# Kernel optimization log

Hardware: AMD Instinct MI355X
Metric: run time of the kernel (lower is better)

The kernel has to match this reference:

```python
import jax, jax.numpy as jnp
import numpy as np

H, D = 4, 32          # heads, per-head dim (= hidden_channels)
HD = H * D            # concat width fed between layers
L = 2                 # num HGT layers
OUT = 128             # final output dim
SCALE = 1.0 / np.sqrt(D)


def _seg_softmax(score, seg, n):
    # segment softmax over incoming edges per destination node, per head
    mx = jax.ops.segment_max(score, seg, num_segments=n)
    ex = jnp.exp(score - mx[seg])
    den = jax.ops.segment_sum(ex, seg, num_segments=n)
    return ex / den[seg]


def _hgt_side(q_dst, k_src, v_src, src, dst, a_rel, m_rel, p_rel, n_dst):
    # k/v: [N_src,H,D]; a_rel,m_rel: [H,D,D]; p_rel: [H]
    k_t = jnp.einsum('ehd,hdf->ehf', k_src[src], a_rel)          # [E,H,D]
    score = (q_dst[dst] * k_t).sum(-1) * p_rel * SCALE           # [E,H]
    alpha = _seg_softmax(score, dst, n_dst)                      # [E,H]
    v_t = jnp.einsum('ehd,hdf->ehf', v_src[src], m_rel)          # [E,H,D]
    return jax.ops.segment_sum(alpha[..., None] * v_t, dst, num_segments=n_dst)


def _forward(x_m, x_g, W_in_m, b_in_m, W_in_g, b_in_g,
             Wk_m, bk_m, Wq_m, bq_m, Wv_m, bv_m,
             Wk_g, bk_g, Wq_g, bq_g, Wv_g, bv_g,
             a_mg, m_mg, p_mg, a_gm, m_gm, p_gm,
             Wa_m, ba_m, Wa_g, ba_g, skip_m, skip_g,
             W_out_m, b_out_m, W_out_g, b_out_g,
             edge_mg_src, edge_mg_dst, edge_gm_src, edge_gm_dst):
    Nm, Ng = x_m.shape[0], x_g.shape[0]
    # per-node-type input projection
    h_m = x_m @ W_in_m + b_in_m                                  # [Nm,HD]
    h_g = x_g @ W_in_g + b_in_g                                  # [Ng,HD]
    for l in range(L):
        k_m = (h_m @ Wk_m[l] + bk_m[l]).reshape(Nm, H, D)
        q_m = (h_m @ Wq_m[l] + bq_m[l]).reshape(Nm, H, D)
        v_m = (h_m @ Wv_m[l] + bv_m[l]).reshape(Nm, H, D)
        k_g = (h_g @ Wk_g[l] + bk_g[l]).reshape(Ng, H, D)
        q_g = (h_g @ Wq_g[l] + bq_g[l]).reshape(Ng, H, D)
        v_g = (h_g @ Wv_g[l] + bv_g[l]).reshape(Ng, H, D)
        agg_g = _hgt_side(q_g, k_m, v_m, edge_mg_src, edge_mg_dst,
                          a_mg[l], m_mg[l], p_mg[l], Ng)         # [Ng,H,D]
        agg_m = _hgt_side(q_m, k_g, v_g, edge_gm_src, edge_gm_dst,
                          a_gm[l], m_gm[l], p_gm[l], Nm)         # [Nm,H,D]
        o_m = jax.nn.gelu(agg_m.reshape(Nm, HD), approximate=False) @ Wa_m[l] + ba_m[l]
        o_g = jax.nn.gelu(agg_g.reshape(Ng, HD), approximate=False) @ Wa_g[l] + ba_g[l]
        bm = jax.nn.sigmoid(skip_m[l])
        bg = jax.nn.sigmoid(skip_g[l])
        h_m = jax.nn.elu(bm * o_m + (1.0 - bm) * h_m)            # HGTConv skip, then model-level ELU
        h_g = jax.nn.elu(bg * o_g + (1.0 - bg) * h_g)
    out_m = h_m @ W_out_m + b_out_m                              # [Nm,OUT]
    out_g = h_g @ W_out_g + b_out_g                              # [Ng,OUT]
    return jnp.concatenate([out_m, out_g], axis=0)               # [Nm+Ng,OUT]


def setup_inputs() -> dict:
    key = jax.random.key(0)
    ks = iter(jax.random.split(key, 64))
    Nm, Ng, E = 100000, 20000, 500000
    Fm, Fg = 20, 50
    def n(shape, s=0.05):
        return jax.random.normal(next(ks), shape, jnp.float32) * s
    inp = {
        'x_m': n((Nm, Fm), 1.0), 'x_g': n((Ng, Fg), 1.0),
        'W_in_m': n((Fm, HD)), 'b_in_m': jnp.zeros((HD,), jnp.float32),
        'W_in_g': n((Fg, HD)), 'b_in_g': jnp.zeros((HD,), jnp.float32),
        'Wk_m': n((L, HD, HD)), 'bk_m': jnp.zeros((L, HD), jnp.float32),
        'Wq_m': n((L, HD, HD)), 'bq_m': jnp.zeros((L, HD), jnp.float32),
        'Wv_m': n((L, HD, HD)), 'bv_m': jnp.zeros((L, HD), jnp.float32),
        'Wk_g': n((L, HD, HD)), 'bk_g': jnp.zeros((L, HD), jnp.float32),
        'Wq_g': n((L, HD, HD)), 'bq_g': jnp.zeros((L, HD), jnp.float32),
        'Wv_g': n((L, HD, HD)), 'bv_g': jnp.zeros((L, HD), jnp.float32),
        'a_mg': n((L, H, D, D)), 'm_mg': n((L, H, D, D)),
        'p_mg': jnp.ones((L, H), jnp.float32),
        'a_gm': n((L, H, D, D)), 'm_gm': n((L, H, D, D)),
        'p_gm': jnp.ones((L, H), jnp.float32),
        'Wa_m': n((L, HD, HD)), 'ba_m': jnp.zeros((L, HD), jnp.float32),
        'Wa_g': n((L, HD, HD)), 'ba_g': jnp.zeros((L, HD), jnp.float32),
        'skip_m': jnp.ones((L,), jnp.float32), 'skip_g': jnp.ones((L,), jnp.float32),
        'W_out_m': n((HD, OUT)), 'b_out_m': jnp.zeros((OUT,), jnp.float32),
        'W_out_g': n((HD, OUT)), 'b_out_g': jnp.zeros((OUT,), jnp.float32),
        'edge_mg_src': jax.random.randint(next(ks), (E,), 0, Nm, jnp.int32),
        'edge_mg_dst': jax.random.randint(next(ks), (E,), 0, Ng, jnp.int32),
        'edge_gm_src': jax.random.randint(next(ks), (E,), 0, Ng, jnp.int32),
        'edge_gm_dst': jax.random.randint(next(ks), (E,), 0, Nm, jnp.int32),
    }
    return inp


def reference(x_m, x_g, W_in_m, b_in_m, W_in_g, b_in_g,
              Wk_m, bk_m, Wq_m, bq_m, Wv_m, bv_m,
              Wk_g, bk_g, Wq_g, bq_g, Wv_g, bv_g,
              a_mg, m_mg, p_mg, a_gm, m_gm, p_gm,
              Wa_m, ba_m, Wa_g, ba_g, skip_m, skip_g,
              W_out_m, b_out_m, W_out_g, b_out_g,
              edge_mg_src, edge_mg_dst, edge_gm_src, edge_gm_dst):
    return _forward(x_m, x_g, W_in_m, b_in_m, W_in_g, b_in_g,
                    Wk_m, bk_m, Wq_m, bq_m, Wv_m, bv_m,
                    Wk_g, bk_g, Wq_g, bq_g, Wv_g, bv_g,
                    a_mg, m_mg, p_mg, a_gm, m_gm, p_gm,
                    Wa_m, ba_m, Wa_g, ba_g, skip_m, skip_g,
                    W_out_m, b_out_m, W_out_g, b_out_g,
                    edge_mg_src, edge_mg_dst, edge_gm_src, edge_gm_dst)
```

## Files before the change

kernel.cpp:

```cpp
#include <hip/hip_runtime.h>
#include <hip/hip_bf16.h>

#define SCALE_F 0.17677669529663688f

typedef __attribute__((ext_vector_type(8)))  short bfrag;
typedef __attribute__((ext_vector_type(16))) float facc;

__device__ __forceinline__ float lo16(unsigned u){ return __uint_as_float(u << 16); }
__device__ __forceinline__ float hi16(unsigned u){ return __uint_as_float(u & 0xffff0000u); }
__device__ __forceinline__ float bu2f(unsigned short u){ return __uint_as_float((unsigned)u << 16); }
__device__ __forceinline__ unsigned short f2bu(float f){
    __hip_bfloat16 h = __float2bfloat16(f);
    return *reinterpret_cast<unsigned short*>(&h);
}
__device__ __forceinline__ void storeC(float* p, float v){ *p = v; }
__device__ __forceinline__ void storeC(__hip_bfloat16* p, float v){ *p = __float2bfloat16(v); }

__global__ void hist_k(const int* __restrict__ dst, int* __restrict__ cnt, int E, int Nd){
    int e = blockIdx.x*256 + threadIdx.x;
    if (e >= E) return;
    int d = dst[e];
    if ((unsigned)d < (unsigned)Nd) atomicAdd(&cnt[d], 1);
}

__global__ void scan_block_k(const int* __restrict__ cnt, int* __restrict__ incl,
                             int* __restrict__ bsum, int N){
    __shared__ int sh[256];
    int tid = threadIdx.x;
    int i = blockIdx.x*256 + tid;
    int v = (i < N) ? cnt[i] : 0;
    sh[tid] = v;
    __syncthreads();
    for (int off = 1; off < 256; off <<= 1){
        int t = (tid >= off) ? sh[tid-off] : 0;
        __syncthreads();
        sh[tid] += t;
        __syncthreads();
    }
    if (i < N) incl[i] = sh[tid];
    if (tid == 255) bsum[blockIdx.x] = sh[255];
}

__global__ void scan_top_k(int* __restrict__ bsum, int nb){
    __shared__ int sh[512];
    int tid = threadIdx.x;
    int v = (tid < nb) ? bsum[tid] : 0;
    sh[tid] = v;
    __syncthreads();
    for (int off = 1; off < 512; off <<= 1){
        int t = (tid >= off) ? sh[tid-off] : 0;
        __syncthreads();
        sh[tid] += t;
        __syncthreads();
    }
    if (tid < nb) bsum[tid] = sh[tid] - v;
}

__global__ void finalize_k(const int* __restrict__ incl, const int* __restrict__ cnt,
                           const int* __restrict__ boff, int* __restrict__ indptr,
                           int N, int E){
    int i = blockIdx.x*256 + threadIdx.x;
    if (i > N) return;
    if (i == N){ indptr[N] = E; return; }
    indptr[i] = boff[i >> 8] + incl[i] - cnt[i];
}

__global__ void scatter_k(const int* __restrict__ src, const int* __restrict__ dst,
                          const int* __restrict__ indptr, int* __restrict__ cur,
                          int* __restrict__ csr, int E, int Nd){
    int e = blockIdx.x*256 + threadIdx.x;
    if (e >= E) return;
    int d = dst[e];
    if ((unsigned)d >= (unsigned)Nd) return;
    int p = indptr[d] + atomicAdd(&cur[d], 1);
    csr[p] = src[e];
}

template<int K>
__global__ __launch_bounds__(128) void in_proj_k(const float* __restrict__ x,
                                                 const float* __restrict__ W,
                                                 const float* __restrict__ b,
                                                 unsigned short* __restrict__ h, int N){
    constexpr int KP4 = (K + 3)/4, KP = KP4*4;
    int j = threadIdx.x;
    float wreg[KP];
    #pragma unroll
    for (int k = 0; k < KP; ++k) wreg[k] = (k < K) ? W[k*128 + j] : 0.f;
    float bj = b[j];
    __shared__ float xs[8][KP];
    for (int base = blockIdx.x*8; base < N; base += gridDim.x*8){
        __syncthreads();
        for (int t = threadIdx.x; t < 8*KP; t += 128){
            int r = t / KP, k = t - r*KP;
            int row = base + r;
            xs[r][k] = (row < N && k < K) ? x[(size_t)row*K + k] : 0.f;
        }
        __syncthreads();
        #pragma unroll
        for (int r = 0; r < 8; ++r){
            int row = base + r;
            if (row >= N) break;
            float acc = bj;
            #pragma unroll
            for (int kk = 0; kk < KP4; ++kk){
                float4 xv = *(const float4*)(&xs[r][kk*4]);
                acc += xv.x*wreg[kk*4] + xv.y*wreg[kk*4+1]
                     + xv.z*wreg[kk*4+2] + xv.w*wreg[kk*4+3];
            }
            h[(size_t)row*128 + j] = f2bu(acc);
        }
    }
}

__global__ __launch_bounds__(128) void build_wf2_k(
    const float* __restrict__ Wq0, const float* __restrict__ bq0,
    const float* __restrict__ Wk0, const float* __restrict__ bk0,
    const float* __restrict__ Wv0, const float* __restrict__ bv0,
    const float* __restrict__ ar0, const float* __restrict__ mr0,
    unsigned short* __restrict__ Wto0, float* __restrict__ bfo0,
    const float* __restrict__ Wq1, const float* __restrict__ bq1,
    const float* __restrict__ Wk1, const float* __restrict__ bk1,
    const float* __restrict__ Wv1, const float* __restrict__ bv1,
    const float* __restrict__ ar1, const float* __restrict__ mr1,
    unsigned short* __restrict__ Wto1, float* __restrict__ bfo1){
    bool sA = (blockIdx.y == 0);
    const float* Wq = sA ? Wq0 : Wq1;  const float* bq = sA ? bq0 : bq1;
    const float* Wk = sA ? Wk0 : Wk1;  const float* bk = sA ? bk0 : bk1;
    const float* Wv = sA ? Wv0 : Wv1;  const float* bvp = sA ? bv0 : bv1;
    const float* ar = sA ? ar0 : ar1;  const float* mr = sA ? mr0 : mr1;
    unsigned short* Wt = sA ? Wto0 : Wto1;
    float* bf = sA ? bfo0 : bfo1;
    int j = blockIdx.x, row = threadIdx.x;
    int part = j >> 7, f = j & 127, hh = f >> 5, ff = f & 31;
    float v;
    if (part == 0) v = Wq[row*128 + f];
    else {
        const float* Wx  = (part == 1) ? Wk : Wv;
        const float* rel = (part == 1) ? ar : mr;
        float s = 0.f;
        #pragma unroll
        for (int d = 0; d < 32; ++d)
            s += Wx[row*128 + hh*32 + d] * rel[hh*1024 + d*32 + ff];
        v = s;
    }
    Wt[(size_t)j*128 + row] = f2bu(v);
    if (row == 0){
        float bb;
        if (part == 0) bb = bq[f];
        else {
            const float* bx  = (part == 1) ? bk : bvp;
            const float* rel = (part == 1) ? ar : mr;
            float s = 0.f;
            for (int d = 0; d < 32; ++d)
                s += bx[hh*32 + d] * rel[hh*1024 + d*32 + ff];
            bb = s;
        }
        bf[j] = bb;
    }
}

__global__ void transpose6_k(const float* a0, const float* a1, const float* a2,
                             const float* a3, const float* a4, const float* a5,
                             unsigned short* d0, unsigned short* d1, unsigned short* d2,
                             unsigned short* d3, unsigned short* d4, unsigned short* d5){
    int y = blockIdx.y;
    const float* S = (y==0)?a0:(y==1)?a1:(y==2)?a2:(y==3)?a3:(y==4)?a4:a5;
    unsigned short* D = (y==0)?d0:(y==1)?d1:(y==2)?d2:(y==3)?d3:(y==4)?d4:d5;
    int idx = blockIdx.x*256 + threadIdx.x;
    int n = idx >> 7, k = idx & 127;
    D[idx] = f2bu(S[k*128 + n]);
}

template<typename CT, int MODE>
__global__ __launch_bounds__(256) void mfma_gemm2(
    const unsigned short* __restrict__ A0, const unsigned short* __restrict__ Wt0,
    const float* __restrict__ bias0, CT* __restrict__ C0, unsigned short* __restrict__ H0,
    int N0, const float* __restrict__ skip0,
    const unsigned short* __restrict__ A1, const unsigned short* __restrict__ Wt1,
    const float* __restrict__ bias1, CT* __restrict__ C1, unsigned short* __restrict__ H1,
    int N1, const float* __restrict__ skip1,
    int ldc, int nblk0){
    bool s0 = ((int)blockIdx.x < nblk0);
    const unsigned short* A  = s0 ? A0 : A1;
    const unsigned short* Wt = s0 ? Wt0 : Wt1;
    const float* bias = s0 ? bias0 : bias1;
    CT* C = s0 ? C0 : C1;
    unsigned short* H = s0 ? H0 : H1;
    int N = s0 ? N0 : N1;
    const float* skip = s0 ? skip0 : skip1;
    int bx = s0 ? blockIdx.x : (blockIdx.x - nblk0);

    __shared__ unsigned short As[64][136];
    __shared__ unsigned short Bs[128][136];
    int tid = threadIdx.x;
    int rb = bx*64, cb = blockIdx.y*128;
    #pragma unroll
    for (int ph = 0; ph < 4; ++ph){
        int c = ph*256 + tid;
        int r = c >> 4, off = (c & 15)*8;
        uint4 v = make_uint4(0,0,0,0);
        if (rb + r < N) v = ((const uint4*)(A + (size_t)(rb + r)*128))[c & 15];
        *(uint4*)(&As[r][off]) = v;
    }
    #pragma unroll
    for (int ph = 0; ph < 8; ++ph){
        int c = ph*256 + tid;
        int r = c >> 4, off = (c & 15)*8;
        uint4 v = ((const uint4*)(Wt + (size_t)(cb + r)*128))[c & 15];
        *(uint4*)(&Bs[r][off]) = v;
    }
    __syncthreads();
    int w = tid >> 6, lane = tid & 63;
    int wr = (w >> 1)*32, wc = (w & 1)*64;
    int m = lane & 31, quad = lane >> 5;
    facc acc0, acc1;
    #pragma unroll
    for (int i = 0; i < 16; ++i){ acc0[i] = 0.f; acc1[i] = 0.f; }
    const unsigned short* ap  = &As[wr + m][quad*8];
    const unsigned short* bp0 = &Bs[wc + m][quad*8];
    const unsigned short* bp1 = &Bs[wc + 32 + m][quad*8];
    #pragma unroll
    for (int kc = 0; kc < 8; ++kc){
        bfrag a  = *(const bfrag*)(ap  + kc*16);
        bfrag b0 = *(const bfrag*)(bp0 + kc*16);
        bfrag b1 = *(const bfrag*)(bp1 + kc*16);
        acc0 = __builtin_amdgcn_mfma_f32_32x32x16_bf16(a, b0, acc0, 0, 0, 0);
        acc1 = __builtin_amdgcn_mfma_f32_32x32x16_bf16(a, b1, acc1, 0, 0, 0);
    }
    int col0 = cb + wc + m, col1 = col0 + 32;
    float bias0v = bias[col0], bias1v = bias[col1];
    float bm = 0.f;
    if (MODE == 2) bm = 1.f/(1.f + __expf(-skip[0]));
    #pragma unroll
    for (int r = 0; r < 16; ++r){
        int lrow = wr + 4*quad + (r & 3) + 8*(r >> 2);
        int grow = rb + lrow;
        if (grow >= N) continue;
        float o0 = acc0[r] + bias0v;
        float o1 = acc1[r] + bias1v;
        if (MODE == 0){
            storeC(&C[(size_t)grow*ldc + col0], o0);
            storeC(&C[(size_t)grow*ldc + col1], o1);
        } else {
            size_t i0 = (size_t)grow*128 + col0, i1 = (size_t)grow*128 + col1;
            float v0 = bm*o0 + (1.f - bm)*bu2f(H[i0]);
            float v1 = bm*o1 + (1.f - bm)*bu2f(H[i1]);
            v0 = (v0 > 0.f) ? v0 : expm1f(v0);
            v1 = (v1 > 0.f) ? v1 : expm1f(v1);
            H[i0] = f2bu(v0);
            H[i1] = f2bu(v1);
        }
    }
}

__global__ __launch_bounds__(256) void edge_attn2_k(
    const int* __restrict__ ipA, const int* __restrict__ csrA,
    const unsigned short* __restrict__ qdA, const unsigned short* __restrict__ qsA,
    const float* __restrict__ pA, unsigned* __restrict__ aggA, int NdA,
    const int* __restrict__ ipB, const int* __restrict__ csrB,
    const unsigned short* __restrict__ qdB, const unsigned short* __restrict__ qsB,
    const float* __restrict__ pB, unsigned* __restrict__ aggB, int NdB,
    int nblkA){
    bool sA = ((int)blockIdx.x < nblkA);
    const int* ip  = sA ? ipA : ipB;
    const int* csr = sA ? csrA : csrB;
    const unsigned* qd = (const unsigned*)(sA ? qdA : qdB);
    const unsigned* qs = (const unsigned*)(sA ? qsA : qsB);
    const float* p = sA ? pA : pB;
    unsigned* agg = sA ? aggA : aggB;
    int Nd = sA ? NdA : NdB;
    int bx = sA ? blockIdx.x : (blockIdx.x - nblkA);
    int wid  = (bx << 2) | (threadIdx.x >> 6);
    int lane = threadIdx.x & 63;
    if (wid >= Nd) return;
    float ph = p[lane >> 4] * SCALE_F;
    unsigned qu = qd[(size_t)wid*192 + lane];
    float q0 = lo16(qu), q1 = hi16(qu);
    int beg = ip[wid], end = ip[wid + 1];
    float den = 0.f, a0 = 0.f, a1 = 0.f;
    int i = beg;
    for (; i + 1 < end; i += 2){
        int s0 = csr[i], s1 = csr[i+1];
        const unsigned* b0 = qs + (size_t)s0*192;
        const unsigned* b1 = qs + (size_t)s1*192;
        unsigned ku0 = b0[64 + lane], vu0 = b0[128 + lane];
        unsigned ku1 = b1[64 + lane], vu1 = b1[128 + lane];
        float t0 = q0*lo16(ku0) + q1*hi16(ku0);
        float t1 = q0*lo16(ku1) + q1*hi16(ku1);
        t0 += __shfl_xor(t0, 1);  t1 += __shfl_xor(t1, 1);
        t0 += __shfl_xor(t0, 2);  t1 += __shfl_xor(t1, 2);
        t0 += __shfl_xor(t0, 4);  t1 += __shfl_xor(t1, 4);
        t0 += __shfl_xor(t0, 8);  t1 += __shfl_xor(t1, 8);
        float e0 = __expf(t0*ph), e1 = __expf(t1*ph);
        den += e0 + e1;
        a0 += e0*lo16(vu0) + e1*lo16(vu1);
        a1 += e0*hi16(vu0) + e1*hi16(vu1);
    }
    if (i < end){
        int s0 = csr[i];
        const unsigned* b0 = qs + (size_t)s0*192;
        unsigned ku0 = b0[64 + lane], vu0 = b0[128 + lane];
        float t0 = q0*lo16(ku0) + q1*hi16(ku0);
        t0 += __shfl_xor(t0, 1);
        t0 += __shfl_xor(t0, 2);
        t0 += __shfl_xor(t0, 4);
        t0 += __shfl_xor(t0, 8);
        float e0 = __expf(t0*ph);
        den += e0; a0 += e0*lo16(vu0); a1 += e0*hi16(vu0);
    }
    float inv = (den > 0.f) ? 1.f/den : 0.f;
    float o0 = a0*inv, o1 = a1*inv;
    o0 = 0.5f*o0*(1.f + erff(o0*0.70710678118654752f));
    o1 = 0.5f*o1*(1.f + erff(o1*0.70710678118654752f));
    agg[(size_t)wid*64 + lane] = (unsigned)f2bu(o0) | ((unsigned)f2bu(o1) << 16);
}

extern "C" void kernel_launch(void* const* d_in, const int* in_sizes, int n_in,
                              void* d_out, int out_size, void* d_ws, size_t ws_size,
                              hipStream_t stream){
    typedef const float* FP;
    FP x_m = (FP)d_in[0], x_g = (FP)d_in[1];
    FP W_in_m = (FP)d_in[2], b_in_m = (FP)d_in[3], W_in_g = (FP)d_in[4], b_in_g = (FP)d_in[5];
    FP Wk_m = (FP)d_in[6],  bk_m = (FP)d_in[7],  Wq_m = (FP)d_in[8],  bq_m = (FP)d_in[9];
    FP Wv_m = (FP)d_in[10], bv_m = (FP)d_in[11];
    FP Wk_g = (FP)d_in[12], bk_g = (FP)d_in[13], Wq_g = (FP)d_in[14], bq_g = (FP)d_in[15];
    FP Wv_g = (FP)d_in[16], bv_g = (FP)d_in[17];
    FP a_mg = (FP)d_in[18], m_mg = (FP)d_in[19], p_mg = (FP)d_in[20];
    FP a_gm = (FP)d_in[21], m_gm = (FP)d_in[22], p_gm = (FP)d_in[23];
    FP Wa_m = (FP)d_in[24], ba_m = (FP)d_in[25], Wa_g = (FP)d_in[26], ba_g = (FP)d_in[27];
    FP skip_m = (FP)d_in[28], skip_g = (FP)d_in[29];
    FP W_out_m = (FP)d_in[30], b_out_m = (FP)d_in[31], W_out_g = (FP)d_in[32], b_out_g = (FP)d_in[33];
    const int* e_mg_src = (const int*)d_in[34];
    const int* e_mg_dst = (const int*)d_in[35];
    const int* e_gm_src = (const int*)d_in[36];
    const int* e_gm_dst = (const int*)d_in[37];

    const int Nm = in_sizes[0] / 20;
    const int Ng = in_sizes[1] / 50;
    const int E1 = in_sizes[34];
    const int E2 = in_sizes[36];

    char* wp = (char*)d_ws;
    auto alloc = [&](size_t bytes) -> char* {
        char* r = wp; wp += (bytes + 255) & ~(size_t)255; return r;
    };
    unsigned short* h_m   = (unsigned short*)alloc((size_t)Nm*128*2);
    unsigned short* h_g   = (unsigned short*)alloc((size_t)Ng*128*2);
    unsigned short* agg_m = (unsigned short*)alloc((size_t)Nm*128*2);
    unsigned short* agg_g = (unsigned short*)alloc((size_t)Ng*128*2);
    unsigned short* qkv_m = (unsigned short*)alloc((size_t)Nm*384*2);
    unsigned short* qkv_g = (unsigned short*)alloc((size_t)Ng*384*2);
    unsigned short* Wtf   = (unsigned short*)alloc((size_t)4*49152*2);
    float*          bfv   = (float*)alloc((size_t)4*384*4);
    unsigned short* Wta   = (unsigned short*)alloc((size_t)4*16384*2);
    unsigned short* Wtout = (unsigned short*)alloc((size_t)2*16384*2);
    int* indptr_g = (int*)alloc((size_t)(Ng+1)*4);
    int* csr_mg   = (int*)alloc((size_t)E1*4);
    int* indptr_m = (int*)alloc((size_t)(Nm+1)*4);
    int* csr_gm   = (int*)alloc((size_t)E2*4);
    int maxN = Nm > Ng ? Nm : Ng;
    int* cnt  = (int*)alloc((size_t)maxN*4);
    int* cur  = (int*)alloc((size_t)maxN*4);
    int* cnt2 = (int*)alloc((size_t)maxN*4);
    int* cur2 = (int*)alloc((size_t)maxN*4);
    int* incl = (int*)alloc((size_t)maxN*4);
    int* bsum = (int*)alloc(512*4);

    size_t used = (size_t)(wp - (char*)d_ws);
    if (used > ws_size){
        hipMemsetAsync(d_out, 0, (size_t)out_size*4, stream);
        return;
    }
    hipMemsetAsync(cnt, 0, (size_t)((char*)cur2 - (char*)cnt) + (size_t)maxN*4, stream);

    auto buildCSR = [&](const int* esrc, const int* edst, int E, int Nd,
                        int* indptr, int* csr, int* c0, int* c1){
        hist_k<<<(E + 255)/256, 256, 0, stream>>>(edst, c0, E, Nd);
        int nb = (Nd + 255)/256;
        scan_block_k<<<nb, 256, 0, stream>>>(c0, incl, bsum, Nd);
        scan_top_k<<<1, 512, 0, stream>>>(bsum, nb);
        finalize_k<<<(Nd + 256)/256 + 1, 256, 0, stream>>>(incl, c0, bsum, indptr, Nd, E);
        scatter_k<<<(E + 255)/256, 256, 0, stream>>>(esrc, edst, indptr, c1, csr, E, Nd);
    };
    buildCSR(e_mg_src, e_mg_dst, E1, Ng, indptr_g, csr_mg, cnt, cur);
    buildCSR(e_gm_src, e_gm_dst, E2, Nm, indptr_m, csr_gm, cnt2, cur2);

    transpose6_k<<<dim3(64, 6), 256, 0, stream>>>(
        Wa_m, Wa_g, Wa_m + 16384, Wa_g + 16384, W_out_m, W_out_g,
        Wta, Wta + 16384, Wta + 32768, Wta + 49152, Wtout, Wtout + 16384);
    for (int l = 0; l < 2; ++l){
        build_wf2_k<<<dim3(384, 2), 128, 0, stream>>>(
            Wq_m + l*16384, bq_m + l*128, Wk_m + l*16384, bk_m + l*128,
            Wv_m + l*16384, bv_m + l*128, a_mg + l*4096, m_mg + l*4096,
            Wtf + (size_t)(l*2+0)*49152, bfv + (l*2+0)*384,
            Wq_g + l*16384, bq_g + l*128, Wk_g + l*16384, bk_g + l*128,
            Wv_g + l*16384, bv_g + l*128, a_gm + l*4096, m_gm + l*4096,
            Wtf + (size_t)(l*2+1)*49152, bfv + (l*2+1)*384);
    }

    int gim = (Nm + 7)/8; if (gim > 2048) gim = 2048;
    int gig = (Ng + 7)/8; if (gig > 2048) gig = 2048;
    in_proj_k<20><<<gim, 128, 0, stream>>>(x_m, W_in_m, b_in_m, h_m, Nm);
    in_proj_k<50><<<gig, 128, 0, stream>>>(x_g, W_in_g, b_in_g, h_g, Ng);

    int gxm = (Nm + 63)/64, gxg = (Ng + 63)/64;
    int nbA = (Ng + 3)/4, nbB = (Nm + 3)/4;

    for (int l = 0; l < 2; ++l){
        mfma_gemm2<__hip_bfloat16, 0><<<dim3(gxm + gxg, 3), 256, 0, stream>>>(
            h_m, Wtf + (size_t)(l*2+0)*49152, bfv + (l*2+0)*384,
            (__hip_bfloat16*)qkv_m, nullptr, Nm, nullptr,
            h_g, Wtf + (size_t)(l*2+1)*49152, bfv + (l*2+1)*384,
            (__hip_bfloat16*)qkv_g, nullptr, Ng, nullptr,
            384, gxm);

        edge_attn2_k<<<nbA + nbB, 256, 0, stream>>>(
            indptr_g, csr_mg, qkv_g, qkv_m, p_mg + l*4, (unsigned*)agg_g, Ng,
            indptr_m, csr_gm, qkv_m, qkv_g, p_gm + l*4, (unsigned*)agg_m, Nm,
            nbA);

        mfma_gemm2<float, 2><<<dim3(gxm + gxg, 1), 256, 0, stream>>>(
            agg_m, Wta + (size_t)(l*2+0)*16384, ba_m + l*128, (float*)nullptr, h_m, Nm, skip_m + l,
            agg_g, Wta + (size_t)(l*2+1)*16384, ba_g + l*128, (float*)nullptr, h_g, Ng, skip_g + l,
            128, gxm);
    }

    float* outp = (float*)d_out;
    mfma_gemm2<float, 0><<<dim3(gxm + gxg, 1), 256, 0, stream>>>(
        h_m, Wtout, b_out_m, outp, nullptr, Nm, nullptr,
        h_g, Wtout + 16384, b_out_g, outp + (size_t)Nm*128, nullptr, Ng, nullptr,
        128, gxm);
}
```

Measured before the change: 657.3 us.

## Process four edges per wavefront with 16-lane groups and 128-bit loads

The edge attention kernel now splits each 64-lane wavefront into four 16-lane slots. Each slot handles a different incoming edge and each lane loads 8 bf16 values with a uint4 load, in place of one edge per wavefront with 32-bit loads per lane. This is meant to raise memory-level parallelism and cut shuffle-reduction depth per edge. The cost is a cross-slot reduction of 9 values at the end and more registers per thread. The output index mapping is rearranged to match the new lane layout.

```diff
diff --git a/kernel.cpp b/kernel.cpp
--- a/kernel.cpp
+++ b/kernel.cpp
@@ -15,6 +15,10 @@
 }
 __device__ __forceinline__ void storeC(float* p, float v){ *p = v; }
 __device__ __forceinline__ void storeC(__hip_bfloat16* p, float v){ *p = __float2bfloat16(v); }
+__device__ __forceinline__ void up8(uint4 v, float* f){
+    f[0]=lo16(v.x); f[1]=hi16(v.x); f[2]=lo16(v.y); f[3]=hi16(v.y);
+    f[4]=lo16(v.z); f[5]=hi16(v.z); f[6]=lo16(v.w); f[7]=hi16(v.w);
+}
 
 __global__ void hist_k(const int* __restrict__ dst, int* __restrict__ cnt, int E, int Nd){
     int e = blockIdx.x*256 + threadIdx.x;
@@ -253,7 +257,7 @@
     }
 }
 
-__global__ __launch_bounds__(256) void edge_attn2_k(
+__global__ __launch_bounds__(256) void edge_attn3_k(
     const int* __restrict__ ipA, const int* __restrict__ csrA,
     const unsigned short* __restrict__ qdA, const unsigned short* __restrict__ qsA,
     const float* __restrict__ pA, unsigned* __restrict__ aggA, int NdA,
@@ -273,46 +277,41 @@
     int wid  = (bx << 2) | (threadIdx.x >> 6);
     int lane = threadIdx.x & 63;
     if (wid >= Nd) return;
-    float ph = p[lane >> 4] * SCALE_F;
-    unsigned qu = qd[(size_t)wid*192 + lane];
-    float q0 = lo16(qu), q1 = hi16(qu);
+    int slot = lane >> 4, j = lane & 15;
+    float ph = p[j >> 2] * SCALE_F;
+    uint4 qv = ((const uint4*)(qd + (size_t)wid*192))[j];
+    float q[8]; up8(qv, q);
     int beg = ip[wid], end = ip[wid + 1];
-    float den = 0.f, a0 = 0.f, a1 = 0.f;
-    int i = beg;
-    for (; i + 1 < end; i += 2){
-        int s0 = csr[i], s1 = csr[i+1];
-        const unsigned* b0 = qs + (size_t)s0*192;
-        const unsigned* b1 = qs + (size_t)s1*192;
-        unsigned ku0 = b0[64 + lane], vu0 = b0[128 + lane];
-        unsigned ku1 = b1[64 + lane], vu1 = b1[128 + lane];
-        float t0 = q0*lo16(ku0) + q1*hi16(ku0);
-        float t1 = q0*lo16(ku1) + q1*hi16(ku1);
-        t0 += __shfl_xor(t0, 1);  t1 += __shfl_xor(t1, 1);
-        t0 += __shfl_xor(t0, 2);  t1 += __shfl_xor(t1, 2);
-        t0 += __shfl_xor(t0, 4);  t1 += __shfl_xor(t1, 4);
-        t0 += __shfl_xor(t0, 8);  t1 += __shfl_xor(t1, 8);
-        float e0 = __expf(t0*ph), e1 = __expf(t1*ph);
-        den += e0 + e1;
-        a0 += e0*lo16(vu0) + e1*lo16(vu1);
-        a1 += e0*hi16(vu0) + e1*hi16(vu1);
-    }
-    if (i < end){
-        int s0 = csr[i];
-        const unsigned* b0 = qs + (size_t)s0*192;
-        unsigned ku0 = b0[64 + lane], vu0 = b0[128 + lane];
-        float t0 = q0*lo16(ku0) + q1*hi16(ku0);
-        t0 += __shfl_xor(t0, 1);
-        t0 += __shfl_xor(t0, 2);
-        t0 += __shfl_xor(t0, 4);
-        t0 += __shfl_xor(t0, 8);
-        float e0 = __expf(t0*ph);
-        den += e0; a0 += e0*lo16(vu0); a1 += e0*hi16(vu0);
+    float den = 0.f;
+    float acc[8] = {0.f,0.f,0.f,0.f,0.f,0.f,0.f,0.f};
+    for (int i = beg + slot; i < end; i += 4){
+        int s = csr[i];
+        const uint4* base = (const uint4*)(qs + (size_t)s*192);
+        uint4 kv = base[16 + j];
+        uint4 vv = base[32 + j];
+        float kf[8]; up8(kv, kf);
+        float part = q[0]*kf[0] + q[1]*kf[1] + q[2]*kf[2] + q[3]*kf[3]
+                   + q[4]*kf[4] + q[5]*kf[5] + q[6]*kf[6] + q[7]*kf[7];
+        part += __shfl_xor(part, 1);
+        part += __shfl_xor(part, 2);
+        float e = __expf(part * ph);
+        float vf[8]; up8(vv, vf);
+        den += e;
+        #pragma unroll
+        for (int d = 0; d < 8; ++d) acc[d] += e * vf[d];
+    }
+    den += __shfl_xor(den, 16);
+    den += __shfl_xor(den, 32);
+    #pragma unroll
+    for (int d = 0; d < 8; ++d){
+        acc[d] += __shfl_xor(acc[d], 16);
+        acc[d] += __shfl_xor(acc[d], 32);
     }
     float inv = (den > 0.f) ? 1.f/den : 0.f;
-    float o0 = a0*inv, o1 = a1*inv;
+    float o0 = acc[2*slot]*inv, o1 = acc[2*slot + 1]*inv;
     o0 = 0.5f*o0*(1.f + erff(o0*0.70710678118654752f));
     o1 = 0.5f*o1*(1.f + erff(o1*0.70710678118654752f));
-    agg[(size_t)wid*64 + lane] = (unsigned)f2bu(o0) | ((unsigned)f2bu(o1) << 16);
+    agg[(size_t)wid*64 + j*4 + slot] = (unsigned)f2bu(o0) | ((unsigned)f2bu(o1) << 16);
 }
 
 extern "C" void kernel_launch(void* const* d_in, const int* in_sizes, int n_in,
@@ -414,7 +413,7 @@
             (__hip_bfloat16*)qkv_g, nullptr, Ng, nullptr,
             384, gxm);
 
-        edge_attn2_k<<<nbA + nbB, 256, 0, stream>>>(
+        edge_attn3_k<<<nbA + nbB, 256, 0, stream>>>(
             indptr_g, csr_mg, qkv_g, qkv_m, p_mg + l*4, (unsigned*)agg_g, Ng,
             indptr_m, csr_gm, qkv_m, qkv_g, p_gm + l*4, (unsigned*)agg_m, Nm,
             nbA);
```

New measurement: 644.8 us. Within noise of the previous version (-1.9%).
